# Kernel tuning notes

Hardware: AMD Instinct MI355X
Metric: run time of the kernel (lower is better)

Reference implementation:

```python
import jax, jax.numpy as jnp
import numpy as np

N = 100000
NEG_SLOPE = 0.2
EPS = 1e-16


def gat_conv(x, edge_index, W, att_src, att_dst, bias, concat):
    # x: [N, Fin]; W: [Fin, H*C]; att_*: [H, C]; edge_index: [2, E] (with self loops)
    H, C = att_src.shape
    src, dst = edge_index[0], edge_index[1]
    h = (x @ W).reshape(-1, H, C)                       # [N, H, C]
    a_src = (h * att_src).sum(-1)                       # [N, H]
    a_dst = (h * att_dst).sum(-1)                       # [N, H]
    e = a_src[src] + a_dst[dst]                         # [E, H]
    e = jnp.where(e >= 0, e, NEG_SLOPE * e)             # LeakyReLU(0.2)
    # segment softmax over destination-node neighborhoods
    m = jax.ops.segment_max(e, dst, num_segments=N)     # [N, H]
    ex = jnp.exp(e - m[dst])
    denom = jax.ops.segment_sum(ex, dst, num_segments=N)
    alpha = ex / (denom[dst] + EPS)                     # [E, H]
    msg = h[src] * alpha[:, :, None]                    # [E, H, C]
    out = jax.ops.segment_sum(msg, dst, num_segments=N)  # [N, H, C]
    out = out.reshape(N, H * C) if concat else out.mean(axis=1)
    return out + bias


def setup_inputs() -> dict:
    key = jax.random.key(0)
    ks = jax.random.split(key, 10)
    Fin, Ch, Co, Hh = 256, 32, 64, 4
    E = 1600000
    x = jax.random.normal(ks[0], (N, Fin), dtype=jnp.float32)
    edge_index = jax.random.randint(ks[1], (2, E), 0, N, dtype=jnp.int64)
    s1 = 1.0 / np.sqrt(Fin)
    s2 = 1.0 / np.sqrt(Hh * Ch)
    W1 = jax.random.normal(ks[2], (Fin, Hh * Ch), dtype=jnp.float32) * s1
    att_src1 = jax.random.normal(ks[3], (Hh, Ch), dtype=jnp.float32) * (1.0 / np.sqrt(Ch))
    att_dst1 = jax.random.normal(ks[4], (Hh, Ch), dtype=jnp.float32) * (1.0 / np.sqrt(Ch))
    b1 = jnp.zeros((Hh * Ch,), dtype=jnp.float32)
    W2 = jax.random.normal(ks[5], (Hh * Ch, Co), dtype=jnp.float32) * s2
    att_src2 = jax.random.normal(ks[6], (1, Co), dtype=jnp.float32) * (1.0 / np.sqrt(Co))
    att_dst2 = jax.random.normal(ks[7], (1, Co), dtype=jnp.float32) * (1.0 / np.sqrt(Co))
    b2 = jnp.zeros((Co,), dtype=jnp.float32)
    return {"x": x, "edge_index": edge_index,
            "W1": W1, "att_src1": att_src1, "att_dst1": att_dst1, "b1": b1,
            "W2": W2, "att_src2": att_src2, "att_dst2": att_dst2, "b2": b2}


def reference(x, edge_index, W1, att_src1, att_dst1, b1, W2, att_src2, att_dst2, b2):
    # add self-loops (PyG GATConv default add_self_loops=True)
    loops = jnp.arange(N, dtype=edge_index.dtype)
    ei = jnp.concatenate([edge_index, jnp.stack([loops, loops])], axis=1)
    h = gat_conv(x, ei, W1, att_src1, att_dst1, b1, concat=True)
    h = jax.nn.elu(h)
    out = gat_conv(h, ei, W2, att_src2, att_dst2, b2, concat=False)
    return out
```

## Files before the change

### kernel.cpp

```cpp
#include <hip/hip_runtime.h>
#include <math.h>

typedef unsigned short ushort_t;
typedef unsigned int uint_t;
typedef __attribute__((ext_vector_type(8))) short short8;
typedef __attribute__((ext_vector_type(4))) float fx4;

__device__ __forceinline__ float bf16_to_f32(ushort_t u) {
    union { uint_t i; float f; } c;
    c.i = ((uint_t)u) << 16;
    return c.f;
}
__device__ __forceinline__ ushort_t f32_to_bf16(float f) {
    union { float f; uint_t i; } c;
    c.f = f;
    const uint_t x = c.i;
    return (ushort_t)((x + 0x7fffu + ((x >> 16) & 1u)) >> 16);
}

__global__ void convT_kernel(const float* __restrict__ W,
                             ushort_t* __restrict__ WT, int k, int m) {
    const int idx = blockIdx.x * 256 + threadIdx.x;
    if (idx >= k * m) return;
    const int mm = idx / k;
    const int kk = idx % k;
    WT[idx] = f32_to_bf16(W[(size_t)kk * m + mm]);
}

template <int TILES, bool A_F32, int K>
__global__ __launch_bounds__(256) void gemm_lds_kernel(
    const void* __restrict__ Avoid, const ushort_t* __restrict__ BT,
    ushort_t* __restrict__ C, int n) {
    constexpr int M = TILES * 16;
    constexpr int CH = K / 8;
    constexpr int NC = K / 32;
    __shared__ ushort_t lds[M * K];
    const int tid = threadIdx.x;

#pragma unroll
    for (int i = 0; i < (M * CH + 255) / 256; ++i) {
        const int idx = tid + i * 256;
        if (idx < M * CH) {
            const int row = idx / CH;
            const int c = idx - row * CH;
            *(short8*)&lds[(size_t)(row * CH + (c ^ (row & 7))) * 8] =
                *(const short8*)(BT + (size_t)row * K + c * 8);
        }
    }
    __syncthreads();

    const int wave = tid >> 6;
    const int lane = tid & 63;
    const int l15 = lane & 15;
    const int quad = lane >> 4;
    const int rowbase = blockIdx.x * 128 + wave * 32;
    const int r0 = min(rowbase + l15, n - 1);
    const int r1 = min(rowbase + 16 + l15, n - 1);
    const size_t off0 = (size_t)r0 * K + quad * 8;
    const size_t off1 = (size_t)r1 * K + quad * 8;

    fx4 acc[2][TILES];
#pragma unroll
    for (int rp = 0; rp < 2; ++rp)
#pragma unroll
        for (int t = 0; t < TILES; ++t) acc[rp][t] = (fx4){0.f, 0.f, 0.f, 0.f};

    fx4 c0a, c0b, c1a, c1b, n0a, n0b, n1a, n1b;
    short8 cb0, cb1, nb0, nb1;

    if constexpr (A_F32) {
        const float* A = (const float*)Avoid;
        c0a = *(const fx4*)(A + off0);
        c0b = *(const fx4*)(A + off0 + 4);
        c1a = *(const fx4*)(A + off1);
        c1b = *(const fx4*)(A + off1 + 4);
    } else {
        const ushort_t* A = (const ushort_t*)Avoid;
        cb0 = *(const short8*)(A + off0);
        cb1 = *(const short8*)(A + off1);
    }

#pragma unroll
    for (int kc = 0; kc < NC; ++kc) {
        if (kc + 1 < NC) {
            const int kd = (kc + 1) * 32;
            if constexpr (A_F32) {
                const float* A = (const float*)Avoid;
                n0a = *(const fx4*)(A + off0 + kd);
                n0b = *(const fx4*)(A + off0 + kd + 4);
                n1a = *(const fx4*)(A + off1 + kd);
                n1b = *(const fx4*)(A + off1 + kd + 4);
            } else {
                const ushort_t* A = (const ushort_t*)Avoid;
                nb0 = *(const short8*)(A + off0 + kd);
                nb1 = *(const short8*)(A + off1 + kd);
            }
        }
        short8 bf[TILES];
#pragma unroll
        for (int t = 0; t < TILES; ++t) {
            const int brow = t * 16 + l15;
            const int c = kc * 4 + quad;
            bf[t] = *(const short8*)&lds[(size_t)(brow * CH +
                                                  (c ^ (brow & 7))) * 8];
        }
        short8 af0, af1;
        if constexpr (A_F32) {
            union { short8 v; ushort_t u[8]; } u0, u1;
#pragma unroll
            for (int j = 0; j < 4; ++j) {
                u0.u[j] = f32_to_bf16(c0a[j]);
                u0.u[4 + j] = f32_to_bf16(c0b[j]);
                u1.u[j] = f32_to_bf16(c1a[j]);
                u1.u[4 + j] = f32_to_bf16(c1b[j]);
            }
            af0 = u0.v;
            af1 = u1.v;
        } else {
            af0 = cb0;
            af1 = cb1;
        }
#pragma unroll
        for (int t = 0; t < TILES; ++t) {
            acc[0][t] = __builtin_amdgcn_mfma_f32_16x16x32_bf16(af0, bf[t],
                                                                acc[0][t],
                                                                0, 0, 0);
            acc[1][t] = __builtin_amdgcn_mfma_f32_16x16x32_bf16(af1, bf[t],
                                                                acc[1][t],
                                                                0, 0, 0);
        }
        if (kc + 1 < NC) {
            if constexpr (A_F32) {
                c0a = n0a; c0b = n0b; c1a = n1a; c1b = n1b;
            } else {
                cb0 = nb0; cb1 = nb1;
            }
        }
    }

#pragma unroll
    for (int rp = 0; rp < 2; ++rp) {
        const int crow0 = rowbase + rp * 16 + quad * 4;
#pragma unroll
        for (int t = 0; t < TILES; ++t) {
#pragma unroll
            for (int r = 0; r < 4; ++r) {
                const int rr = crow0 + r;
                if (rr < n)
                    C[(size_t)rr * M + t * 16 + l15] =
                        f32_to_bf16(acc[rp][t][r]);
            }
        }
    }
}

template <int H, int C>
__global__ void att_kernel(const ushort_t* __restrict__ h,
                           const float* __restrict__ att_s,
                           const float* __restrict__ att_d,
                           float* __restrict__ as_, float* __restrict__ ad_,
                           int n) {
    const int idx = blockIdx.x * blockDim.x + threadIdx.x;
    if (idx >= n * H) return;
    const int node = idx / H;
    const int hh = idx % H;
    const ushort_t* hp = h + (size_t)node * H * C + hh * C;
    float s0 = 0.f, s1 = 0.f;
#pragma unroll
    for (int c = 0; c < C; ++c) {
        const float v = bf16_to_f32(hp[c]);
        s0 += v * att_s[hh * C + c];
        s1 += v * att_d[hh * C + c];
    }
    as_[idx] = s0;
    ad_[idx] = s1;
}

__global__ __launch_bounds__(1024) void hist_kernel(const int* __restrict__ dst,
                                                    int* __restrict__ histG,
                                                    int e, int chunk, int NB,
                                                    int G) {
    __shared__ int hl[512];
    for (int b = threadIdx.x; b < NB; b += 1024) hl[b] = 0;
    __syncthreads();
    const int g = blockIdx.x;
    const int lo = g * chunk;
    const int hi = min(lo + chunk, e);
    for (int i = lo + threadIdx.x; i < hi; i += 1024)
        atomicAdd(&hl[dst[i] >> 8], 1);
    __syncthreads();
    for (int b = threadIdx.x; b < NB; b += 1024) histG[b * G + g] = hl[b];
}

__global__ __launch_bounds__(1024) void scan1_kernel(const int* __restrict__ in,
                                                     int* __restrict__ out,
                                                     int* __restrict__ sums,
                                                     int n) {
    __shared__ int s[1024];
    const int t = threadIdx.x;
    const int i = blockIdx.x * 1024 + t;
    const int v = (i < n) ? in[i] : 0;
    s[t] = v;
    __syncthreads();
    for (int d = 1; d < 1024; d <<= 1) {
        const int x = (t >= d) ? s[t - d] : 0;
        __syncthreads();
        s[t] += x;
        __syncthreads();
    }
    if (i < n) out[i] = s[t] - v;
    if (t == 1023) sums[blockIdx.x] = s[1023];
}

__global__ __launch_bounds__(128) void scan2_kernel(int* sums, int nb) {
    __shared__ int s[128];
    const int t = threadIdx.x;
    const int v = (t < nb) ? sums[t] : 0;
    s[t] = v;
    __syncthreads();
    for (int d = 1; d < 128; d <<= 1) {
        const int x = (t >= d) ? s[t - d] : 0;
        __syncthreads();
        s[t] += x;
        __syncthreads();
    }
    if (t < nb) sums[t] = s[t] - v;
}

__global__ __launch_bounds__(1024) void scan3_kernel(int* __restrict__ out,
                                                     const int* __restrict__ sums,
                                                     int n) {
    const int i = blockIdx.x * 1024 + threadIdx.x;
    if (i < n) out[i] += sums[blockIdx.x];
}

__global__ __launch_bounds__(1024) void bin_kernel(const int* __restrict__ src,
                                                   const int* __restrict__ dst,
                                                   const int* __restrict__ base,
                                                   int2* __restrict__ binned,
                                                   int e, int chunk, int NB,
                                                   int G) {
    __shared__ int cur[512];
    const int g = blockIdx.x;
    for (int b = threadIdx.x; b < NB; b += 1024) cur[b] = base[b * G + g];
    __syncthreads();
    const int lo = g * chunk;
    const int hi = min(lo + chunk, e);
    for (int i = lo + threadIdx.x; i < hi; i += 1024) {
        const int d = dst[i];
        const int p = atomicAdd(&cur[d >> 8], 1);
        binned[p] = make_int2(src[i], d);
    }
}

#define BUILD_CAP 6144
__global__ __launch_bounds__(256) void build_kernel(
    const int2* __restrict__ binned, const int* __restrict__ base,
    int* __restrict__ csr, int* __restrict__ deg, int* __restrict__ offs,
    int e, int n, int NB, int G) {
    __shared__ int2 ep[BUILD_CAP];
    __shared__ int degL[256];
    __shared__ int offL[256];
    __shared__ int curL[256];
    const int b = blockIdx.x;
    const int tid = threadIdx.x;
    const int start = base[b * G];
    const int end = (b == NB - 1) ? e : base[(b + 1) * G];
    const int cnt = end - start;
    const bool stage = (cnt <= BUILD_CAP);
    degL[tid] = 0;
    if (stage)
        for (int i = tid; i < cnt; i += 256) ep[i] = binned[start + i];
    __syncthreads();
    if (stage) {
        for (int i = tid; i < cnt; i += 256) atomicAdd(&degL[ep[i].y & 255], 1);
    } else {
        for (int i = tid; i < cnt; i += 256)
            atomicAdd(&degL[binned[start + i].y & 255], 1);
    }
    __syncthreads();
    const int v = degL[tid];
    offL[tid] = v;
    __syncthreads();
    for (int d = 1; d < 256; d <<= 1) {
        const int x = (tid >= d) ? offL[tid - d] : 0;
        __syncthreads();
        offL[tid] += x;
        __syncthreads();
    }
    const int excl = offL[tid] - v;
    curL[tid] = excl;
    const int node = (b << 8) + tid;
    if (node < n) {
        deg[node] = v;
        offs[node] = start + excl;
    }
    __syncthreads();
    if (stage) {
        for (int i = tid; i < cnt; i += 256) {
            const int p = atomicAdd(&curL[ep[i].y & 255], 1);
            csr[start + p] = ep[i].x;
        }
    } else {
        for (int i = tid; i < cnt; i += 256) {
            const int2 pr = binned[start + i];
            const int p = atomicAdd(&curL[pr.y & 255], 1);
            csr[start + p] = pr.x;
        }
    }
}

template <int H, int C, bool DO_ELU, bool OUT_BF16>
__global__ __launch_bounds__(64) void agg_kernel(
    const ushort_t* __restrict__ h, const float* __restrict__ a_src,
    const float* __restrict__ a_dst, const int* __restrict__ csr,
    const int* __restrict__ offs, const int* __restrict__ deg,
    const float* __restrict__ bias, void* __restrict__ outv, int n) {
    constexpr int HC = H * C;
    constexpr int R = HC / 64;
    constexpr int U = 8;
    const int dst = blockIdx.x;
    const int lane = threadIdx.x;
    const int start = offs[dst];
    const int d = deg[dst];
    const int ch0 = lane * R;
    const int hh = ch0 / C;
    const int myh = hh;
    const float advm = a_dst[dst * H + myh];
    float acc0 = 0.f, acc1 = 0.f;
    float L = 0.f;

    {
        float e = a_src[dst * H + myh] + advm;
        e = fmaxf(e, 0.2f * e);
        const float p = __expf(e);
        L += p;
        const ushort_t* hp = h + (size_t)dst * HC + ch0;
        if (R == 2) {
            const uint_t v = *(const uint_t*)hp;
            acc0 += p * bf16_to_f32((ushort_t)(v & 0xffffu));
            acc1 += p * bf16_to_f32((ushort_t)(v >> 16));
        } else {
            acc0 += p * bf16_to_f32(hp[0]);
        }
    }

    int j = 0;
    for (; j + U <= d; j += U) {
        int sv[U];
#pragma unroll
        for (int u = 0; u < U; ++u) sv[u] = csr[start + j + u];
        int ss[U];
#pragma unroll
        for (int u = 0; u < U; ++u)
            ss[u] = __builtin_amdgcn_readfirstlane(sv[u]);
        float es[U];
#pragma unroll
        for (int u = 0; u < U; ++u) es[u] = a_src[sv[u] * H + myh];
        uint_t hv[U];
#pragma unroll
        for (int u = 0; u < U; ++u) {
            const ushort_t* hp = h + (size_t)ss[u] * HC + ch0;
            if (R == 2) hv[u] = *(const uint_t*)hp;
            else hv[u] = (uint_t)(*hp);
        }
#pragma unroll
        for (int u = 0; u < U; ++u) {
            float e = es[u] + advm;
            e = fmaxf(e, 0.2f * e);
            const float p = __expf(e);
            L += p;
            if (R == 2) {
                acc0 += p * bf16_to_f32((ushort_t)(hv[u] & 0xffffu));
                acc1 += p * bf16_to_f32((ushort_t)(hv[u] >> 16));
            } else {
                acc0 += p * bf16_to_f32((ushort_t)hv[u]);
            }
        }
    }
    for (; j < d; ++j) {
        const int sv = csr[start + j];
        const int ss = __builtin_amdgcn_readfirstlane(sv);
        float e = a_src[sv * H + myh] + advm;
        e = fmaxf(e, 0.2f * e);
        const float p = __expf(e);
        L += p;
        const ushort_t* hp = h + (size_t)ss * HC + ch0;
        if (R == 2) {
            const uint_t v = *(const uint_t*)hp;
            acc0 += p * bf16_to_f32((ushort_t)(v & 0xffffu));
            acc1 += p * bf16_to_f32((ushort_t)(v >> 16));
        } else {
            acc0 += p * bf16_to_f32(hp[0]);
        }
    }

    const float linv = 1.f / (L + 1e-16f);
    float r0 = acc0 * linv + bias[ch0];
    if (DO_ELU) r0 = (r0 > 0.f) ? r0 : (__expf(r0) - 1.f);
    if (R == 2) {
        float r1 = acc1 * linv + bias[ch0 + 1];
        if (DO_ELU) r1 = (r1 > 0.f) ? r1 : (__expf(r1) - 1.f);
        if (OUT_BF16) {
            const uint_t packed =
                (uint_t)f32_to_bf16(r0) | ((uint_t)f32_to_bf16(r1) << 16);
            *(uint_t*)((ushort_t*)outv + (size_t)dst * HC + ch0) = packed;
        } else {
            *(float2*)((float*)outv + (size_t)dst * HC + ch0) =
                make_float2(r0, r1);
        }
    } else {
        if (OUT_BF16)
            ((ushort_t*)outv)[(size_t)dst * HC + ch0] = f32_to_bf16(r0);
        else
            ((float*)outv)[(size_t)dst * HC + ch0] = r0;
    }
}

extern "C" void kernel_launch(void* const* d_in, const int* in_sizes, int n_in,
                              void* d_out, int out_size, void* d_ws,
                              size_t ws_size, hipStream_t stream) {
    const float* x = (const float*)d_in[0];
    const int* ei = (const int*)d_in[1];
    const float* W1 = (const float*)d_in[2];
    const float* att_s1 = (const float*)d_in[3];
    const float* att_d1 = (const float*)d_in[4];
    const float* b1 = (const float*)d_in[5];
    const float* W2 = (const float*)d_in[6];
    const float* att_s2 = (const float*)d_in[7];
    const float* att_d2 = (const float*)d_in[8];
    const float* b2 = (const float*)d_in[9];

    const int N = in_sizes[0] / 256;
    const int E = in_sizes[1] / 2;
    const int* srcp = ei;
    const int* dstp = ei + E;

    const int NB = (N + 255) >> 8;
    const int G = 128;
    const int NBG = NB * G;
    const int chunk = (E + G - 1) / G;
    const int nbs = (NBG + 1023) / 1024;

    float* as1 = (float*)d_ws;
    float* ad1 = as1 + (size_t)N * 4;
    float* as2 = ad1 + (size_t)N * 4;
    float* ad2 = as2 + N;
    int* histG = (int*)(ad2 + N);
    int* base = histG + NBG;
    int* sums = base + NBG;
    int* deg = sums + 128;
    int* offs = deg + N;
    int* csr = offs + N;
    int2* binned = (int2*)(csr + E);
    ushort_t* h1 = (ushort_t*)binned;
    ushort_t* h2 = h1 + (size_t)N * 128;
    ushort_t* h1p = h2 + (size_t)N * 64;
    ushort_t* W1T = h1p + (size_t)N * 128;
    ushort_t* W2T = W1T + 128 * 256;

    convT_kernel<<<(256 * 128 + 255) / 256, 256, 0, stream>>>(W1, W1T, 256, 128);
    convT_kernel<<<(128 * 64 + 255) / 256, 256, 0, stream>>>(W2, W2T, 128, 64);

    hist_kernel<<<G, 1024, 0, stream>>>(dstp, histG, E, chunk, NB, G);
    scan1_kernel<<<nbs, 1024, 0, stream>>>(histG, base, sums, NBG);
    scan2_kernel<<<1, 128, 0, stream>>>(sums, nbs);
    scan3_kernel<<<nbs, 1024, 0, stream>>>(base, sums, NBG);
    bin_kernel<<<G, 1024, 0, stream>>>(srcp, dstp, base, binned, E, chunk, NB,
                                       G);
    build_kernel<<<NB, 256, 0, stream>>>(binned, base, csr, deg, offs, E, N,
                                         NB, G);

    const int gblk = (N + 127) / 128;

    gemm_lds_kernel<8, true, 256><<<gblk, 256, 0, stream>>>(x, W1T, h1, N);
    att_kernel<4, 32><<<(N * 4 + 255) / 256, 256, 0, stream>>>(h1, att_s1,
                                                               att_d1, as1,
                                                               ad1, N);
    agg_kernel<4, 32, true, true><<<N, 64, 0, stream>>>(h1, as1, ad1, csr,
                                                        offs, deg, b1, h1p, N);

    gemm_lds_kernel<4, false, 128><<<gblk, 256, 0, stream>>>(h1p, W2T, h2, N);
    att_kernel<1, 64><<<(N + 255) / 256, 256, 0, stream>>>(h2, att_s2, att_d2,
                                                           as2, ad2, N);
    agg_kernel<1, 64, false, false><<<N, 64, 0, stream>>>(h2, as2, ad2, csr,
                                                          offs, deg, b2, d_out,
                                                          N);
}
```

Measured before the change: 409.5 us.

## Pack four destination nodes per wavefront in aggregation with wide vector loads

The aggregation kernel now gives each 16-lane group its own destination node, so one 64-lane wavefront handles four destinations, and each lane covers 8 or 4 channels using 128-bit or 64-bit loads. This replaces one wavefront per node with a single 2-channel lane slice, which wasted lanes and issued many small gathers. In exchange, all four groups loop to the largest degree among them, masking inactive iterations. The unroll drops to 4, and scalar readfirstlane addressing gives way to per-lane vector addresses.

After: 394.3 us. 3.7% less time.

```diff
diff --git a/kernel.cpp b/kernel.cpp
--- a/kernel.cpp
+++ b/kernel.cpp
@@ -5,6 +5,8 @@
 typedef unsigned int uint_t;
 typedef __attribute__((ext_vector_type(8))) short short8;
 typedef __attribute__((ext_vector_type(4))) float fx4;
+typedef __attribute__((ext_vector_type(4))) uint_t uintx4;
+typedef __attribute__((ext_vector_type(2))) uint_t uintx2;
 
 __device__ __forceinline__ float bf16_to_f32(ushort_t u) {
     union { uint_t i; float f; } c;
@@ -16,6 +18,14 @@
     c.f = f;
     const uint_t x = c.i;
     return (ushort_t)((x + 0x7fffu + ((x >> 16) & 1u)) >> 16);
+}
+__device__ __forceinline__ void unpack_fma(uint_t w, float p, float& a0,
+                                           float& a1) {
+    union { uint_t i; float f; } lo, hi;
+    lo.i = w << 16;
+    hi.i = w & 0xffff0000u;
+    a0 += p * lo.f;
+    a1 += p * hi.f;
 }
 
 __global__ void convT_kernel(const float* __restrict__ W,
@@ -317,103 +327,110 @@
     const int* __restrict__ offs, const int* __restrict__ deg,
     const float* __restrict__ bias, void* __restrict__ outv, int n) {
     constexpr int HC = H * C;
-    constexpr int R = HC / 64;
-    constexpr int U = 8;
-    const int dst = blockIdx.x;
+    constexpr int R = HC / 16;
+    constexpr int RW = R / 2;
+    constexpr int U = 4;
     const int lane = threadIdx.x;
-    const int start = offs[dst];
-    const int d = deg[dst];
-    const int ch0 = lane * R;
-    const int hh = ch0 / C;
-    const int myh = hh;
-    const float advm = a_dst[dst * H + myh];
-    float acc0 = 0.f, acc1 = 0.f;
+    const int s = lane & 15;
+    const int g = lane >> 4;
+    const int dst = blockIdx.x * 4 + g;
+    const int dstc = min(dst, n - 1);
+    const int start = offs[dstc];
+    const int dg = deg[dstc];
+    const int ch0 = s * R;
+    const int myh = (H > 1) ? (ch0 / C) : 0;
+    const float advm = a_dst[dstc * H + myh];
+
+    int dmax = dg;
+    dmax = max(dmax, __shfl_xor(dmax, 16));
+    dmax = max(dmax, __shfl_xor(dmax, 32));
+    dmax = __builtin_amdgcn_readfirstlane(dmax);
+
+    float acc[R];
+#pragma unroll
+    for (int r = 0; r < R; ++r) acc[r] = 0.f;
     float L = 0.f;
 
     {
-        float e = a_src[dst * H + myh] + advm;
+        float e = a_src[dstc * H + myh] + advm;
         e = fmaxf(e, 0.2f * e);
         const float p = __expf(e);
         L += p;
-        const ushort_t* hp = h + (size_t)dst * HC + ch0;
-        if (R == 2) {
-            const uint_t v = *(const uint_t*)hp;
-            acc0 += p * bf16_to_f32((ushort_t)(v & 0xffffu));
-            acc1 += p * bf16_to_f32((ushort_t)(v >> 16));
+        const ushort_t* hp = h + (size_t)((uint_t)dstc * HC) + ch0;
+        if constexpr (RW == 4) {
+            const uintx4 v = *(const uintx4*)hp;
+#pragma unroll
+            for (int w = 0; w < 4; ++w)
+                unpack_fma(v[w], p, acc[2 * w], acc[2 * w + 1]);
         } else {
-            acc0 += p * bf16_to_f32(hp[0]);
-        }
-    }
-
-    int j = 0;
-    for (; j + U <= d; j += U) {
+            const uintx2 v = *(const uintx2*)hp;
+#pragma unroll
+            for (int w = 0; w < 2; ++w)
+                unpack_fma(v[w], p, acc[2 * w], acc[2 * w + 1]);
+        }
+    }
+
+    const int dm1c = (dg > 0) ? dg - 1 : 0;
+
+    for (int j0 = 0; j0 < dmax; j0 += U) {
         int sv[U];
 #pragma unroll
-        for (int u = 0; u < U; ++u) sv[u] = csr[start + j + u];
-        int ss[U];
-#pragma unroll
         for (int u = 0; u < U; ++u)
-            ss[u] = __builtin_amdgcn_readfirstlane(sv[u]);
+            sv[u] = csr[start + min(j0 + u, dm1c)];
         float es[U];
 #pragma unroll
         for (int u = 0; u < U; ++u) es[u] = a_src[sv[u] * H + myh];
-        uint_t hv[U];
+        uint_t hv[U][RW];
 #pragma unroll
         for (int u = 0; u < U; ++u) {
-            const ushort_t* hp = h + (size_t)ss[u] * HC + ch0;
-            if (R == 2) hv[u] = *(const uint_t*)hp;
-            else hv[u] = (uint_t)(*hp);
-        }
+            const ushort_t* hp = h + (size_t)((uint_t)sv[u] * HC) + ch0;
+            if constexpr (RW == 4) {
+                const uintx4 v = *(const uintx4*)hp;
+#pragma unroll
+                for (int w = 0; w < 4; ++w) hv[u][w] = v[w];
+            } else {
+                const uintx2 v = *(const uintx2*)hp;
+#pragma unroll
+                for (int w = 0; w < 2; ++w) hv[u][w] = v[w];
+            }
+        }
+        float p[U];
 #pragma unroll
         for (int u = 0; u < U; ++u) {
             float e = es[u] + advm;
             e = fmaxf(e, 0.2f * e);
-            const float p = __expf(e);
-            L += p;
-            if (R == 2) {
-                acc0 += p * bf16_to_f32((ushort_t)(hv[u] & 0xffffu));
-                acc1 += p * bf16_to_f32((ushort_t)(hv[u] >> 16));
-            } else {
-                acc0 += p * bf16_to_f32((ushort_t)hv[u]);
-            }
-        }
-    }
-    for (; j < d; ++j) {
-        const int sv = csr[start + j];
-        const int ss = __builtin_amdgcn_readfirstlane(sv);
-        float e = a_src[sv * H + myh] + advm;
-        e = fmaxf(e, 0.2f * e);
-        const float p = __expf(e);
-        L += p;
-        const ushort_t* hp = h + (size_t)ss * HC + ch0;
-        if (R == 2) {
-            const uint_t v = *(const uint_t*)hp;
-            acc0 += p * bf16_to_f32((ushort_t)(v & 0xffffu));
-            acc1 += p * bf16_to_f32((ushort_t)(v >> 16));
-        } else {
-            acc0 += p * bf16_to_f32(hp[0]);
-        }
-    }
-
+            const float pe = __expf(e);
+            p[u] = (j0 + u < dg) ? pe : 0.f;
+        }
+#pragma unroll
+        for (int u = 0; u < U; ++u) {
+            L += p[u];
+#pragma unroll
+            for (int w = 0; w < RW; ++w)
+                unpack_fma(hv[u][w], p[u], acc[2 * w], acc[2 * w + 1]);
+        }
+    }
+
+    if (dst >= n) return;
     const float linv = 1.f / (L + 1e-16f);
-    float r0 = acc0 * linv + bias[ch0];
-    if (DO_ELU) r0 = (r0 > 0.f) ? r0 : (__expf(r0) - 1.f);
-    if (R == 2) {
-        float r1 = acc1 * linv + bias[ch0 + 1];
-        if (DO_ELU) r1 = (r1 > 0.f) ? r1 : (__expf(r1) - 1.f);
-        if (OUT_BF16) {
-            const uint_t packed =
-                (uint_t)f32_to_bf16(r0) | ((uint_t)f32_to_bf16(r1) << 16);
-            *(uint_t*)((ushort_t*)outv + (size_t)dst * HC + ch0) = packed;
-        } else {
-            *(float2*)((float*)outv + (size_t)dst * HC + ch0) =
-                make_float2(r0, r1);
-        }
+    float r[R];
+#pragma unroll
+    for (int d = 0; d < R; ++d) {
+        r[d] = acc[d] * linv + bias[ch0 + d];
+        if (DO_ELU) r[d] = (r[d] > 0.f) ? r[d] : (__expf(r[d]) - 1.f);
+    }
+    if constexpr (OUT_BF16) {
+        uintx4 o;
+#pragma unroll
+        for (int w = 0; w < 4; ++w)
+            o[w] = (uint_t)f32_to_bf16(r[2 * w]) |
+                   ((uint_t)f32_to_bf16(r[2 * w + 1]) << 16);
+        *(uintx4*)((ushort_t*)outv + (size_t)dst * HC + ch0) = o;
     } else {
-        if (OUT_BF16)
-            ((ushort_t*)outv)[(size_t)dst * HC + ch0] = f32_to_bf16(r0);
-        else
-            ((float*)outv)[(size_t)dst * HC + ch0] = r0;
+        fx4 o;
+#pragma unroll
+        for (int d = 0; d < 4; ++d) o[d] = r[d];
+        *(fx4*)((float*)outv + (size_t)dst * HC + ch0) = o;
     }
 }
 
@@ -472,18 +489,20 @@
                                          NB, G);
 
     const int gblk = (N + 127) / 128;
+    const int ablk = (N + 3) / 4;
 
     gemm_lds_kernel<8, true, 256><<<gblk, 256, 0, stream>>>(x, W1T, h1, N);
     att_kernel<4, 32><<<(N * 4 + 255) / 256, 256, 0, stream>>>(h1, att_s1,
                                                                att_d1, as1,
                                                                ad1, N);
-    agg_kernel<4, 32, true, true><<<N, 64, 0, stream>>>(h1, as1, ad1, csr,
-                                                        offs, deg, b1, h1p, N);
+    agg_kernel<4, 32, true, true><<<ablk, 64, 0, stream>>>(h1, as1, ad1, csr,
+                                                           offs, deg, b1, h1p,
+                                                           N);
 
     gemm_lds_kernel<4, false, 128><<<gblk, 256, 0, stream>>>(h1p, W2T, h2, N);
     att_kernel<1, 64><<<(N + 255) / 256, 256, 0, stream>>>(h2, att_s2, att_d2,
                                                            as2, ad2, N);
-    agg_kernel<1, 64, false, false><<<N, 64, 0, stream>>>(h2, as2, ad2, csr,
-                                                          offs, deg, b2, d_out,
-                                                          N);
-}
+    agg_kernel<1, 64, false, false><<<ablk, 64, 0, stream>>>(h2, as2, ad2,
+                                                             csr, offs, deg,
+                                                             b2, d_out, N);
+}
```
